# Kernel tuning notes

Hardware: AMD Instinct MI355X
Metric: run time of the kernel (lower is better)

The kernel has to match this reference:

```python
import jax, jax.numpy as jnp
import numpy as np

BASE = 512  # per-axis encoding base; coords and queries are all < 512
NEG_FILL = -1000.0


def _encode(c):
    # c: [..., 4] int32 coords laid out as (x, y, z, batch)
    c = c.astype(jnp.int32)
    # max key = 3*512^3 + 511*(512^2+512+1) < 2^31, fits int32
    return ((c[..., 3] * BASE + c[..., 0]) * BASE + c[..., 1]) * BASE + c[..., 2]


def setup_inputs() -> dict:
    G, B, N, C, M_cap = 128, 4, 400000, 64, 360000
    rng = np.random.default_rng(0)
    # unique active voxels in a B x G^3 grid (torchsparse assumes unique coords)
    flat = rng.choice(B * G * G * G, size=N, replace=False)
    b = flat // (G * G * G)
    rem = flat % (G * G * G)
    x = rem // (G * G)
    y = (rem // G) % G
    z = rem % G
    coords = np.stack([x, y, z, b], axis=1).astype(np.int32)
    # spdownsample(stride=2, minkowski): unique floor-divided coords
    coarse = coords.copy()
    coarse[:, :3] //= 2
    out = np.unique(coarse, axis=0)
    if out.shape[0] >= M_cap:
        out = out[:M_cap]
    else:
        # pad with sentinel coords that can never match any input voxel
        pad = np.full((M_cap - out.shape[0], 4), 255, dtype=np.int32)
        pad[:, 3] = 0
        out = np.concatenate([out, pad], axis=0)
    feats = jax.random.normal(jax.random.key(0), (N, C), dtype=jnp.float32)
    return {
        "coords": jnp.asarray(coords),
        "feats": feats,
        "out_coords": jnp.asarray(out.astype(np.int32)),
    }


def reference(coords, feats, out_coords):
    N = coords.shape[0]
    M = out_coords.shape[0]
    # --- sphash(input.coords): sorted key table for exact-match lookup ---
    keys_in = _encode(coords)                      # [N]
    order = jnp.argsort(keys_in)                   # [N]
    skeys = keys_in[order]                         # [N] sorted
    # --- get_kernel_offsets(2,1,1): the 8 corners of the 2x2x2 kernel ---
    offs = jnp.stack(
        jnp.meshgrid(jnp.arange(2), jnp.arange(2), jnp.arange(2), indexing="ij"),
        axis=-1,
    ).reshape(8, 3)                                 # [8,3] in {0,1}^3
    # --- sphash(out_coords*2 + offsets) ---
    q_xyz = out_coords[None, :, :3] * 2 + offs[:, None, :]          # [8,M,3]
    q_b = jnp.broadcast_to(out_coords[None, :, 3:4], (8, M, 1))     # [8,M,1]
    kq = _encode(jnp.concatenate([q_xyz, q_b], axis=-1))            # [8,M]
    # --- sphashquery: index of matching input coord, -1 if missing ---
    pos = jnp.searchsorted(skeys, kq)              # [8,M]
    posc = jnp.clip(pos, 0, N - 1)
    valid = (pos < N) & (skeys[posc] == kq)
    results = jnp.where(valid, order[posc], -1)    # [8,M]
    # --- gather with -1000 sentinel row, max over the 8 kernel taps ---
    feat_pad = jnp.concatenate(
        [jnp.full((1, feats.shape[1]), NEG_FILL, feats.dtype), feats], axis=0
    )
    out_feature = jnp.max(feat_pad[results + 1], axis=0)  # [M,C]
    return out_feature
```

## Files before the change

kernel.cpp:

```cpp
#include <hip/hip_runtime.h>

#define NEG_FILL -1000.0f
#define ROWS 4


__global__ void scatter_direct(const int* __restrict__ coords,
                               int* __restrict__ table, int N) {
    int i = blockIdx.x * blockDim.x + threadIdx.x;
    if (i >= N) return;
    const int4 c = reinterpret_cast<const int4*>(coords)[i];
    int key = ((c.w * 128 + c.x) * 128 + c.y) * 128 + c.z;
    table[key] = i;
}

__global__ __launch_bounds__(256) void pool_direct(
        const int* __restrict__ out_coords,
        const float* __restrict__ feats,
        const int* __restrict__ table,
        float* __restrict__ out, int M, int Q) {
    int tid  = blockIdx.x * blockDim.x + threadIdx.x;
    int slot = tid >> 3;
    if (slot >= Q) return;
    int lane = threadIdx.x & 63;
    int o    = lane & 7;
    int grp  = lane & 56;
    int off  = ((o >> 2) << 14) + (((o >> 1) & 1) << 7) + (o & 1);

    int  row[ROWS];
    int4 oc[ROWS];
    #pragma unroll
    for (int r = 0; r < ROWS; ++r) {
        row[r] = slot + r * Q;
        int rr = row[r] < M ? row[r] : 0;
        oc[r] = reinterpret_cast<const int4*>(out_coords)[rr];
    }

    int  e[ROWS];
    bool rowok[ROWS];
    #pragma unroll
    for (int r = 0; r < ROWS; ++r) {
        int bx = oc[r].x * 2, by = oc[r].y * 2, bz = oc[r].z * 2, b = oc[r].w;
        rowok[r] = ((unsigned)(bx | by | bz) < 128u) && (row[r] < M);
        int base = ((b * 128 + bx) * 128 + by) * 128 + bz;
        base = rowok[r] ? base : 0;
        e[r] = table[base + off];
    }

    #pragma unroll
    for (int r = 0; r < ROWS; ++r) {
        unsigned long long bal = __ballot(rowok[r] && (e[r] >= 0));
        unsigned m = (unsigned)(bal >> grp) & 0xFFu;

        float4 a0 = make_float4(NEG_FILL, NEG_FILL, NEG_FILL, NEG_FILL);
        float4 a1 = a0;
        while (m) {
            int oo = __ffs(m) - 1;
            m &= m - 1;
            int idx = __shfl(e[r], grp + oo);
            const float4* fp = reinterpret_cast<const float4*>(
                feats + ((long)idx << 6));
            float4 v0 = fp[o];
            float4 v1 = fp[8 + o];
            a0.x = fmaxf(a0.x, v0.x); a0.y = fmaxf(a0.y, v0.y);
            a0.z = fmaxf(a0.z, v0.z); a0.w = fmaxf(a0.w, v0.w);
            a1.x = fmaxf(a1.x, v1.x); a1.y = fmaxf(a1.y, v1.y);
            a1.z = fmaxf(a1.z, v1.z); a1.w = fmaxf(a1.w, v1.w);
        }
        if (row[r] < M) {
            float4* op = reinterpret_cast<float4*>(out + ((long)row[r] << 6));
            op[o]     = a0;
            op[8 + o] = a1;
        }
    }
}


#define HCAP (1 << 20)
#define HMASK (HCAP - 1)

__global__ void scatter_hash(const int* __restrict__ coords,
                             int* __restrict__ hkeys, int* __restrict__ hvals,
                             int N) {
    int i = blockIdx.x * blockDim.x + threadIdx.x;
    if (i >= N) return;
    const int4 c = reinterpret_cast<const int4*>(coords)[i];
    int key = ((c.w * 128 + c.x) * 128 + c.y) * 128 + c.z;
    unsigned slot = ((unsigned)key * 2654435761u) & HMASK;
    while (true) {
        int prev = atomicCAS(&hkeys[slot], -1, key);
        if (prev == -1 || prev == key) { hvals[slot] = i; break; }
        slot = (slot + 1) & HMASK;
    }
}

__device__ __forceinline__ int hash_lookup(const int* __restrict__ hkeys,
                                           const int* __restrict__ hvals,
                                           int key) {
    unsigned slot = ((unsigned)key * 2654435761u) & HMASK;
    while (true) {
        int k = hkeys[slot];
        if (k == key) return hvals[slot];
        if (k == -1) return -1;
        slot = (slot + 1) & HMASK;
    }
}

__global__ void pool_hash(const int* __restrict__ out_coords,
                          const float* __restrict__ feats,
                          const int* __restrict__ hkeys,
                          const int* __restrict__ hvals,
                          float* __restrict__ out, int M) {
    int tid = blockIdx.x * blockDim.x + threadIdx.x;
    int row = tid >> 4;
    if (row >= M) return;
    int cg = (tid & 15) << 2;

    const int4 oc = reinterpret_cast<const int4*>(out_coords)[row];
    int bx = oc.x * 2, by = oc.y * 2, bz = oc.z * 2, b = oc.w;

    float4 acc = make_float4(NEG_FILL, NEG_FILL, NEG_FILL, NEG_FILL);

    if ((unsigned)(bx | by | bz) < 128u) {
        int base = ((b * 128 + bx) * 128 + by) * 128 + bz;
        #pragma unroll
        for (int o = 0; o < 8; ++o) {
            int key = base + (o >> 2) * (128 * 128) + ((o >> 1) & 1) * 128 + (o & 1);
            int idx = hash_lookup(hkeys, hvals, key);
            if (idx >= 0) {
                const float4 v = *reinterpret_cast<const float4*>(
                    feats + ((long)idx << 6) + cg);
                acc.x = fmaxf(acc.x, v.x);
                acc.y = fmaxf(acc.y, v.y);
                acc.z = fmaxf(acc.z, v.z);
                acc.w = fmaxf(acc.w, v.w);
            }
        }
    }
    *reinterpret_cast<float4*>(out + ((long)row << 6) + cg) = acc;
}

extern "C" void kernel_launch(void* const* d_in, const int* in_sizes, int n_in,
                              void* d_out, int out_size, void* d_ws, size_t ws_size,
                              hipStream_t stream) {
    const int*   coords     = (const int*)d_in[0];
    const float* feats      = (const float*)d_in[1];
    const int*   out_coords = (const int*)d_in[2];
    float*       out        = (float*)d_out;

    int N = in_sizes[0] / 4;
    int M = in_sizes[2] / 4;

    const size_t TABLE_BYTES = (size_t)4 * 128 * 128 * 128 * sizeof(int);

    if (ws_size >= TABLE_BYTES) {
        int* table = (int*)d_ws;
        hipMemsetAsync(table, 0xFF, TABLE_BYTES, stream);
        scatter_direct<<<(N + 255) / 256, 256, 0, stream>>>(coords, table, N);
        int Q = (M + ROWS - 1) / ROWS;
        int threads = Q * 8;
        pool_direct<<<(threads + 255) / 256, 256, 0, stream>>>(
            out_coords, feats, table, out, M, Q);
    } else {
        int* hkeys = (int*)d_ws;
        int* hvals = hkeys + HCAP;
        hipMemsetAsync(hkeys, 0xFF, (size_t)HCAP * sizeof(int), stream);
        scatter_hash<<<(N + 255) / 256, 256, 0, stream>>>(coords, hkeys, hvals, N);
        pool_hash<<<((M * 16) + 255) / 256, 256, 0, stream>>>(
            out_coords, feats, hkeys, hvals, out, M);
    }
}
```

Measured before the change: 57.43 us.

## Drop dense table memset by validating lookups against input coords

Removes the full-grid memset of the dense lookup table and instead checks each table entry by re-reading the input coordinate it points to and comparing its key with the query key, so stale workspace contents are rejected. This avoids writing the whole table on every call, at the cost of one extra coordinate gather per tap. Output stores also become nontemporal. Correctness depends on the entry range check and key verification, which do filter garbage from uninitialised memory.

Result: faster. 54.79 us (-4.6%).

```diff
diff --git a/kernel.cpp b/kernel.cpp
--- a/kernel.cpp
+++ b/kernel.cpp
@@ -2,6 +2,8 @@
 
 #define NEG_FILL -1000.0f
 #define ROWS 4
+
+typedef float nfloat4 __attribute__((ext_vector_type(4)));
 
 
 __global__ void scatter_direct(const int* __restrict__ coords,
@@ -16,8 +18,9 @@
 __global__ __launch_bounds__(256) void pool_direct(
         const int* __restrict__ out_coords,
         const float* __restrict__ feats,
+        const int* __restrict__ coords,
         const int* __restrict__ table,
-        float* __restrict__ out, int M, int Q) {
+        float* __restrict__ out, int M, int N, int Q) {
     int tid  = blockIdx.x * blockDim.x + threadIdx.x;
     int slot = tid >> 3;
     if (slot >= Q) return;
@@ -36,6 +39,7 @@
     }
 
     int  e[ROWS];
+    int  qkey[ROWS];
     bool rowok[ROWS];
     #pragma unroll
     for (int r = 0; r < ROWS; ++r) {
@@ -43,12 +47,23 @@
         rowok[r] = ((unsigned)(bx | by | bz) < 128u) && (row[r] < M);
         int base = ((b * 128 + bx) * 128 + by) * 128 + bz;
         base = rowok[r] ? base : 0;
-        e[r] = table[base + off];
+        qkey[r] = base + off;
+        e[r] = table[qkey[r]];
+    }
+
+    bool val[ROWS];
+    #pragma unroll
+    for (int r = 0; r < ROWS; ++r) {
+        bool eok = (unsigned)e[r] < (unsigned)N;
+        int  es  = eok ? e[r] : 0;
+        const int4 c = reinterpret_cast<const int4*>(coords)[es];
+        int vkey = ((c.w * 128 + c.x) * 128 + c.y) * 128 + c.z;
+        val[r] = rowok[r] && eok && (vkey == qkey[r]);
     }
 
     #pragma unroll
     for (int r = 0; r < ROWS; ++r) {
-        unsigned long long bal = __ballot(rowok[r] && (e[r] >= 0));
+        unsigned long long bal = __ballot(val[r]);
         unsigned m = (unsigned)(bal >> grp) & 0xFFu;
 
         float4 a0 = make_float4(NEG_FILL, NEG_FILL, NEG_FILL, NEG_FILL);
@@ -67,9 +82,9 @@
             a1.z = fmaxf(a1.z, v1.z); a1.w = fmaxf(a1.w, v1.w);
         }
         if (row[r] < M) {
-            float4* op = reinterpret_cast<float4*>(out + ((long)row[r] << 6));
-            op[o]     = a0;
-            op[8 + o] = a1;
+            nfloat4* op = reinterpret_cast<nfloat4*>(out + ((long)row[r] << 6));
+            __builtin_nontemporal_store(*reinterpret_cast<nfloat4*>(&a0), op + o);
+            __builtin_nontemporal_store(*reinterpret_cast<nfloat4*>(&a1), op + 8 + o);
         }
     }
 }
@@ -154,16 +169,15 @@
 
     if (ws_size >= TABLE_BYTES) {
         int* table = (int*)d_ws;
-        hipMemsetAsync(table, 0xFF, TABLE_BYTES, stream);
         scatter_direct<<<(N + 255) / 256, 256, 0, stream>>>(coords, table, N);
         int Q = (M + ROWS - 1) / ROWS;
         int threads = Q * 8;
         pool_direct<<<(threads + 255) / 256, 256, 0, stream>>>(
-            out_coords, feats, table, out, M, Q);
+            out_coords, feats, coords, table, out, M, N, Q);
     } else {
         int* hkeys = (int*)d_ws;
         int* hvals = hkeys + HCAP;
-        hipMemsetAsync(hkeys, 0xFF, (size_t)HCAP * sizeof(int), stream);
+        (void)hipMemsetAsync(hkeys, 0xFF, (size_t)HCAP * sizeof(int), stream);
         scatter_hash<<<(N + 255) / 256, 256, 0, stream>>>(coords, hkeys, hvals, N);
         pool_hash<<<((M * 16) + 255) / 256, 256, 0, stream>>>(
             out_coords, feats, hkeys, hvals, out, M);
```
